# Optimization experiments

Measured on AMD Instinct MI355X. Metric: run time of the kernel, lower is better.

## Reference

```python
import jax, jax.numpy as jnp
import numpy as np

N = 16000   # query points
M = 16000   # support points
NB = 32     # neighbors per query
A = 4       # kanchor (SO(2)/z-axis discrete anchors, kanchor<10 branch)
K = 15      # kernel points
CIN = 32
COUT = 32
RADIUS = 1.0
KP_EXTENT = 0.6


def _make_kernel_points(key):
    # KPConv-style kernel points inside a sphere of radius 0.66*RADIUS, first point at center
    kp = jax.random.normal(key, (K, 3), dtype=jnp.float32)
    kp = kp / (jnp.linalg.norm(kp, axis=-1, keepdims=True) + 1e-8)
    r = jax.random.uniform(jax.random.fold_in(key, 1), (K, 1), dtype=jnp.float32) ** (1.0 / 3.0)
    kp = kp * r * (0.66 * RADIUS)
    return kp.at[0].set(0.0)


def _make_anchors():
    # kanchor=4 -> rotations about z by 2*pi*a/A (E2PN get_anchors for kanchor<10)
    ang = 2.0 * jnp.pi * jnp.arange(A, dtype=jnp.float32) / A
    c, s = jnp.cos(ang), jnp.sin(ang)
    z = jnp.zeros_like(c)
    o = jnp.ones_like(c)
    return jnp.stack([c, -s, z, s, c, z, z, z, o], axis=-1).reshape(A, 3, 3)


def setup_inputs() -> dict:
    key = jax.random.key(0)
    k1, k2, k3, k4, k5, k6 = jax.random.split(key, 6)
    q_pts = jax.random.uniform(k1, (N, 3), dtype=jnp.float32) * 0.5
    s_pts = jax.random.uniform(k2, (M, 3), dtype=jnp.float32) * 0.5
    neighb_inds = jax.random.randint(k3, (N, NB), 0, M, dtype=jnp.int32)
    x = jax.random.normal(k4, (M, A, CIN), dtype=jnp.float32)
    kernel_points = _make_kernel_points(k5)
    anchors = _make_anchors()
    # kaiming-uniform-ish init of the (K, C_in, C_out) separable conv weights
    bound = float(np.sqrt(6.0 / ((1 + 5) * CIN)))
    weights = jax.random.uniform(k6, (K, CIN, COUT), dtype=jnp.float32,
                                 minval=-bound, maxval=bound)
    return {"q_pts": q_pts, "s_pts": s_pts, "neighb_inds": neighb_inds, "x": x,
            "kernel_points": kernel_points, "anchors": anchors, "weights": weights}


def reference(q_pts, s_pts, neighb_inds, x, kernel_points, anchors, weights):
    # neighbor gather, centered on query points: [N, NB, 3]
    neighbors = s_pts[neighb_inds] - q_pts[:, None, :]
    # rotate kernel points by each anchor: [A, K, 3]
    rot_kp = jnp.einsum('aij,kj->aki', anchors, kernel_points)
    # squared distances via |n|^2 + |kp|^2 - 2 n.kp (avoids [A,N,NB,K,3] blowup)
    n2 = jnp.sum(neighbors * neighbors, axis=-1)          # [N, NB]
    k2 = jnp.sum(rot_kp * rot_kp, axis=-1)                # [A, K]
    cross = jnp.einsum('nbj,akj->anbk', neighbors, rot_kp)
    sq_distances = n2[None, :, :, None] + k2[:, None, None, :] - 2.0 * cross  # [A,N,NB,K]
    # linear KP influence, clamped at 0
    all_weights = jnp.clip(1.0 - jnp.sqrt(jnp.maximum(sq_distances, 1e-12)) / KP_EXTENT,
                           0.0, None)                      # [A, N, NB, K]
    # gather neighbor features: [N, NB, A, C_in]
    neighb_x = x[neighb_inds]
    # weight neighbors onto kernel points (sum aggregation): [A, N, K, C_in]
    weighted_feats = jnp.einsum('anbk,nbac->ankc', all_weights, neighb_x)
    # per-kernel-point small GEMMs, summed over K: [N, A, C_out]
    out = jnp.einsum('ankc,kcd->nad', weighted_feats, weights)
    return out
```

## Files before the change

### kernel.cpp

```cpp
#include <hip/hip_runtime.h>


typedef short bf16x8 __attribute__((ext_vector_type(8)));
typedef float f32x4  __attribute__((ext_vector_type(4)));

__device__ __forceinline__ unsigned short f2bf(float f) {
    unsigned u = __builtin_bit_cast(unsigned, f);
    return (unsigned short)((u + 0x8000u) >> 16);
}

__device__ __forceinline__ unsigned pack2bf(float hi, float lo) {
    unsigned uh = __builtin_bit_cast(unsigned, hi) + 0x8000u;
    unsigned ul = __builtin_bit_cast(unsigned, lo) + 0x8000u;
    return __builtin_amdgcn_perm(uh, ul, 0x07060302u);
}

__global__ void prep_w(const float* __restrict__ W, unsigned short* __restrict__ Wp) {
    const int idx = blockIdx.x * 256 + threadIdx.x;
    const int kk = idx >> 10, d = (idx >> 5) & 31, e = idx & 31;
    const int kcs = kk * 32 + e;
    const int c = kcs >> 4, k = kcs & 15;
    const float v = (k < 15) ? W[(k * 32 + c) * 32 + d] : 0.0f;
    Wp[idx] = f2bf(v);
}

__global__ void prep_x(const float* __restrict__ x, unsigned short* __restrict__ xb) {
    const int i = (blockIdx.x * 256 + threadIdx.x) * 8;
    const float4 v0 = *(const float4*)&x[i];
    const float4 v1 = *(const float4*)&x[i + 4];
    uint4 u;
    u.x = pack2bf(v0.y, v0.x); u.y = pack2bf(v0.w, v0.z);
    u.z = pack2bf(v1.y, v1.x); u.w = pack2bf(v1.w, v1.z);
    *(uint4*)&xb[i] = u;
}

__global__ __launch_bounds__(256) void kpconv_mfma(
    const float* __restrict__ q_pts,
    const float* __restrict__ s_pts,
    const int*   __restrict__ inds,
    const unsigned short* __restrict__ xb,
    const float* __restrict__ kp,
    const float* __restrict__ anchors,
    const unsigned short* __restrict__ Wp,
    float*       __restrict__ out)
{
    __shared__ __align__(16) unsigned short xa_s[16384];
    __shared__ __align__(16) float nbr[576];
    __shared__ __align__(16) float rk_s[256];

    const int t  = threadIdx.x;
    const int n0 = blockIdx.x * 4;

    {
        const int c4 = t & 7, bg = (t >> 3) & 7, q = t >> 6;
        const int4 rows = *(const int4*)&inds[(n0 + q) * 32 + 4 * bg];
        const int fc  = c4 & 3;
        const int bb  = 4 * (bg & 1);
        const int blk = 8 * ((bg >> 1) ^ fc);
        unsigned short* base = &xa_s[(q * 32) * 32 + blk + bb];
        #pragma unroll
        for (int a = 0; a < 4; ++a) {
            const uint2 r0 = *(const uint2*)&xb[rows.x * 128 + a * 32 + c4 * 4];
            const uint2 r1 = *(const uint2*)&xb[rows.y * 128 + a * 32 + c4 * 4];
            const uint2 r2 = *(const uint2*)&xb[rows.z * 128 + a * 32 + c4 * 4];
            const uint2 r3 = *(const uint2*)&xb[rows.w * 128 + a * 32 + c4 * 4];
            unsigned short* pa = base + a * 4096;
            uint2 w;
            w.x = __builtin_amdgcn_perm(r1.x, r0.x, 0x05040100u);
            w.y = __builtin_amdgcn_perm(r3.x, r2.x, 0x05040100u);
            *(uint2*)&pa[(4 * c4 + 0) * 32] = w;
            w.x = __builtin_amdgcn_perm(r1.x, r0.x, 0x07060302u);
            w.y = __builtin_amdgcn_perm(r3.x, r2.x, 0x07060302u);
            *(uint2*)&pa[(4 * c4 + 1) * 32] = w;
            w.x = __builtin_amdgcn_perm(r1.y, r0.y, 0x05040100u);
            w.y = __builtin_amdgcn_perm(r3.y, r2.y, 0x05040100u);
            *(uint2*)&pa[(4 * c4 + 2) * 32] = w;
            w.x = __builtin_amdgcn_perm(r1.y, r0.y, 0x07060302u);
            w.y = __builtin_amdgcn_perm(r3.y, r2.y, 0x07060302u);
            *(uint2*)&pa[(4 * c4 + 3) * 32] = w;
        }
    }

    if (t < 128) {
        const int q = t >> 5, b = t & 31;
        const int idx = inds[(n0 + q) * 32 + b];
        const float qx = q_pts[(n0 + q) * 3 + 0];
        const float qy = q_pts[(n0 + q) * 3 + 1];
        const float qz = q_pts[(n0 + q) * 3 + 2];
        const float nx = s_pts[idx * 3 + 0] - qx;
        const float ny = s_pts[idx * 3 + 1] - qy;
        const float nz = s_pts[idx * 3 + 2] - qz;
        float4 v; v.x = nx; v.y = ny; v.z = nz; v.w = nx*nx + ny*ny + nz*nz;
        *(float4*)&nbr[(q * 36 + b + (b >> 3)) * 4] = v;
    } else if (t < 192) {
        const int j = t - 128;
        const int a = j >> 4, k = j & 15;
        float4 v;
        if (k < 15) {
            const float kx = kp[k*3+0], ky = kp[k*3+1], kz = kp[k*3+2];
            const float* R = anchors + a * 9;
            v.x = R[0]*kx + R[1]*ky + R[2]*kz;
            v.y = R[3]*kx + R[4]*ky + R[5]*kz;
            v.z = R[6]*kx + R[7]*ky + R[8]*kz;
            v.w = v.x*v.x + v.y*v.y + v.z*v.z;
        } else {
            v.x = 0.0f; v.y = 0.0f; v.z = 0.0f; v.w = 1e30f;
        }
        *(float4*)&rk_s[(a * 16 + k) * 4] = v;
    }
    __syncthreads();

    const int a    = t >> 6;
    const int lane = t & 63;
    const int l15  = lane & 15;
    const int quad = lane >> 4;
    const int fc   = (l15 >> 2) & 3;

    const float4 r4 = *(const float4*)&rk_s[(a * 16 + l15) * 4];
    unsigned short* wfb = &xa_s[a * 4096];

    #pragma unroll
    for (int q = 0; q < 4; ++q) {
        float w8[8];
        #pragma unroll
        for (int j = 0; j < 8; ++j) {
            const int b = quad * 8 + j;
            const float4 nb = *(const float4*)&nbr[(q * 36 + b + (b >> 3)) * 4];
            const float dot = fmaf(nb.x, r4.x, fmaf(nb.y, r4.y, nb.z * r4.z));
            const float sq  = fmaf(-2.0f, dot, nb.w + r4.w);
            const float d   = sqrtf(fmaxf(sq, 1e-12f));
            w8[j] = fmaxf(fmaf(d, -(1.0f / 0.6f), 1.0f), 0.0f);
        }
        uint4 uu;
        uu.x = pack2bf(w8[1], w8[0]); uu.y = pack2bf(w8[3], w8[2]);
        uu.z = pack2bf(w8[5], w8[4]); uu.w = pack2bf(w8[7], w8[6]);
        const bf16x8 afr = __builtin_bit_cast(bf16x8, uu);

        const bf16x8 b0 = *(const bf16x8*)&xa_s[((a*4 + q)*32 + l15)      * 32 + 8 * (quad ^ fc)];
        const bf16x8 b1 = *(const bf16x8*)&xa_s[((a*4 + q)*32 + l15 + 16) * 32 + 8 * (quad ^ fc)];
        f32x4 d0 = {0.f,0.f,0.f,0.f}, d1 = {0.f,0.f,0.f,0.f};
        d0 = __builtin_amdgcn_mfma_f32_16x16x32_bf16(afr, b0, d0, 0, 0, 0);
        d1 = __builtin_amdgcn_mfma_f32_16x16x32_bf16(afr, b1, d1, 0, 0, 0);
        uint2 s0, s1;
        s0.x = pack2bf(d0[1], d0[0]); s0.y = pack2bf(d0[3], d0[2]);
        s1.x = pack2bf(d1[1], d1[0]); s1.y = pack2bf(d1[3], d1[2]);
        *(uint2*)&wfb[q*512 + (( l15       * 16 + quad * 4) ^ (q * 16))] = s0;
        *(uint2*)&wfb[q*512 + (((l15 + 16) * 16 + quad * 4) ^ (q * 16))] = s1;
    }

    const int qq = l15 & 3;
    f32x4 o0 = {0.f,0.f,0.f,0.f}, o1 = {0.f,0.f,0.f,0.f};
    #pragma unroll
    for (int kk = 0; kk < 16; ++kk) {
        const bf16x8 a2 = *(const bf16x8*)&wfb[qq*512 + ((kk*32 + quad*8) ^ (qq*16))];
        const bf16x8 w0 = *(const bf16x8*)&Wp[kk*1024 + l15*32 + quad*8];
        const bf16x8 w1 = *(const bf16x8*)&Wp[kk*1024 + (l15+16)*32 + quad*8];
        o0 = __builtin_amdgcn_mfma_f32_16x16x32_bf16(a2, w0, o0, 0, 0, 0);
        o1 = __builtin_amdgcn_mfma_f32_16x16x32_bf16(a2, w1, o1, 0, 0, 0);
    }
    if (quad == 0) {
        #pragma unroll
        for (int r = 0; r < 4; ++r) {
            out[((n0 + r) * 4 + a) * 32 + l15]      = o0[r];
            out[((n0 + r) * 4 + a) * 32 + 16 + l15] = o1[r];
        }
    }
}

extern "C" void kernel_launch(void* const* d_in, const int* in_sizes, int n_in,
                              void* d_out, int out_size, void* d_ws, size_t ws_size,
                              hipStream_t stream) {
    const float* q_pts   = (const float*)d_in[0];
    const float* s_pts   = (const float*)d_in[1];
    const int*   inds    = (const int*)d_in[2];
    const float* x       = (const float*)d_in[3];
    const float* kp      = (const float*)d_in[4];
    const float* anchors = (const float*)d_in[5];
    const float* weights = (const float*)d_in[6];
    float*       out     = (float*)d_out;

    unsigned short* Wp = (unsigned short*)d_ws;
    unsigned short* xb = (unsigned short*)((char*)d_ws + (1 << 16));

    prep_w<<<dim3(64),   dim3(256), 0, stream>>>(weights, Wp);
    prep_x<<<dim3(1000), dim3(256), 0, stream>>>(x, xb);
    kpconv_mfma<<<dim3(4000), dim3(256), 0, stream>>>(
        q_pts, s_pts, inds, xb, kp, anchors, Wp, out);
}
```

Measured before the change: 123.8 us.

## Process four query groups per block with register-prefetched gathers

Each block now handles 16 query points in four groups of four. The neighbor-feature and point gathers for the next group are issued into registers before the current group's MFMA work, so global gather latency overlaps compute. The rotated kernel points are computed once per block, and the grid shrinks from 4000 to 1000 blocks. The trade-offs are higher register pressure from the 16-entry prefetch buffer, fewer blocks to spread across CUs, and an extra barrier per group.

```diff
diff --git a/kernel.cpp b/kernel.cpp
--- a/kernel.cpp
+++ b/kernel.cpp
@@ -48,57 +48,24 @@
     __shared__ __align__(16) float nbr[576];
     __shared__ __align__(16) float rk_s[256];
 
-    const int t  = threadIdx.x;
-    const int n0 = blockIdx.x * 4;
-
-    {
-        const int c4 = t & 7, bg = (t >> 3) & 7, q = t >> 6;
-        const int4 rows = *(const int4*)&inds[(n0 + q) * 32 + 4 * bg];
-        const int fc  = c4 & 3;
-        const int bb  = 4 * (bg & 1);
-        const int blk = 8 * ((bg >> 1) ^ fc);
-        unsigned short* base = &xa_s[(q * 32) * 32 + blk + bb];
-        #pragma unroll
-        for (int a = 0; a < 4; ++a) {
-            const uint2 r0 = *(const uint2*)&xb[rows.x * 128 + a * 32 + c4 * 4];
-            const uint2 r1 = *(const uint2*)&xb[rows.y * 128 + a * 32 + c4 * 4];
-            const uint2 r2 = *(const uint2*)&xb[rows.z * 128 + a * 32 + c4 * 4];
-            const uint2 r3 = *(const uint2*)&xb[rows.w * 128 + a * 32 + c4 * 4];
-            unsigned short* pa = base + a * 4096;
-            uint2 w;
-            w.x = __builtin_amdgcn_perm(r1.x, r0.x, 0x05040100u);
-            w.y = __builtin_amdgcn_perm(r3.x, r2.x, 0x05040100u);
-            *(uint2*)&pa[(4 * c4 + 0) * 32] = w;
-            w.x = __builtin_amdgcn_perm(r1.x, r0.x, 0x07060302u);
-            w.y = __builtin_amdgcn_perm(r3.x, r2.x, 0x07060302u);
-            *(uint2*)&pa[(4 * c4 + 1) * 32] = w;
-            w.x = __builtin_amdgcn_perm(r1.y, r0.y, 0x05040100u);
-            w.y = __builtin_amdgcn_perm(r3.y, r2.y, 0x05040100u);
-            *(uint2*)&pa[(4 * c4 + 2) * 32] = w;
-            w.x = __builtin_amdgcn_perm(r1.y, r0.y, 0x07060302u);
-            w.y = __builtin_amdgcn_perm(r3.y, r2.y, 0x07060302u);
-            *(uint2*)&pa[(4 * c4 + 3) * 32] = w;
-        }
-    }
-
-    if (t < 128) {
-        const int q = t >> 5, b = t & 31;
-        const int idx = inds[(n0 + q) * 32 + b];
-        const float qx = q_pts[(n0 + q) * 3 + 0];
-        const float qy = q_pts[(n0 + q) * 3 + 1];
-        const float qz = q_pts[(n0 + q) * 3 + 2];
-        const float nx = s_pts[idx * 3 + 0] - qx;
-        const float ny = s_pts[idx * 3 + 1] - qy;
-        const float nz = s_pts[idx * 3 + 2] - qz;
-        float4 v; v.x = nx; v.y = ny; v.z = nz; v.w = nx*nx + ny*ny + nz*nz;
-        *(float4*)&nbr[(q * 36 + b + (b >> 3)) * 4] = v;
-    } else if (t < 192) {
+    const int t    = threadIdx.x;
+    const int nblk = blockIdx.x * 16;
+
+    const int c4 = t & 7, bg = (t >> 3) & 7, qg = t >> 6;
+    const int a = t >> 6, lane = t & 63, l15 = lane & 15, quad = lane >> 4;
+    const int fc = (l15 >> 2) & 3;
+
+    uint2 gb[16];
+    int   pidx = 0;
+    float psx = 0, psy = 0, psz = 0, pqx = 0, pqy = 0, pqz = 0;
+
+    if (t >= 128 && t < 192) {
         const int j = t - 128;
-        const int a = j >> 4, k = j & 15;
+        const int aa = j >> 4, k = j & 15;
         float4 v;
         if (k < 15) {
             const float kx = kp[k*3+0], ky = kp[k*3+1], kz = kp[k*3+2];
-            const float* R = anchors + a * 9;
+            const float* R = anchors + aa * 9;
             v.x = R[0]*kx + R[1]*ky + R[2]*kz;
             v.y = R[3]*kx + R[4]*ky + R[5]*kz;
             v.z = R[6]*kx + R[7]*ky + R[8]*kz;
@@ -106,64 +73,128 @@
         } else {
             v.x = 0.0f; v.y = 0.0f; v.z = 0.0f; v.w = 1e30f;
         }
-        *(float4*)&rk_s[(a * 16 + k) * 4] = v;
+        *(float4*)&rk_s[(aa * 16 + k) * 4] = v;
     }
-    __syncthreads();
-
-    const int a    = t >> 6;
-    const int lane = t & 63;
-    const int l15  = lane & 15;
-    const int quad = lane >> 4;
-    const int fc   = (l15 >> 2) & 3;
-
-    const float4 r4 = *(const float4*)&rk_s[(a * 16 + l15) * 4];
-    unsigned short* wfb = &xa_s[a * 4096];
+    {
+        const int4 rows = *(const int4*)&inds[(nblk + qg) * 32 + 4 * bg];
+        #pragma unroll
+        for (int aa = 0; aa < 4; ++aa) {
+            gb[aa*4+0] = *(const uint2*)&xb[rows.x * 128 + aa * 32 + c4 * 4];
+            gb[aa*4+1] = *(const uint2*)&xb[rows.y * 128 + aa * 32 + c4 * 4];
+            gb[aa*4+2] = *(const uint2*)&xb[rows.z * 128 + aa * 32 + c4 * 4];
+            gb[aa*4+3] = *(const uint2*)&xb[rows.w * 128 + aa * 32 + c4 * 4];
+        }
+        if (t < 128) {
+            const int qq2 = t >> 5, b = t & 31;
+            pidx = inds[(nblk + qq2) * 32 + b];
+            psx = s_pts[pidx*3+0]; psy = s_pts[pidx*3+1]; psz = s_pts[pidx*3+2];
+            pqx = q_pts[(nblk+qq2)*3+0]; pqy = q_pts[(nblk+qq2)*3+1]; pqz = q_pts[(nblk+qq2)*3+2];
+        }
+    }
 
     #pragma unroll
-    for (int q = 0; q < 4; ++q) {
-        float w8[8];
+    for (int g = 0; g < 4; ++g) {
+        const int n0 = nblk + g * 4;
+
+        if (t < 128) {
+            const int qq2 = t >> 5, b = t & 31;
+            const float nx = psx - pqx, ny = psy - pqy, nz = psz - pqz;
+            float4 v; v.x = nx; v.y = ny; v.z = nz; v.w = nx*nx + ny*ny + nz*nz;
+            *(float4*)&nbr[(qq2 * 36 + b + (b >> 3)) * 4] = v;
+        }
+        {
+            const int bb  = 4 * (bg & 1);
+            const int blk = 8 * ((bg >> 1) ^ (c4 & 3));
+            unsigned short* base = &xa_s[(qg * 32) * 32 + blk + bb];
+            #pragma unroll
+            for (int aa = 0; aa < 4; ++aa) {
+                unsigned short* pa = base + aa * 4096;
+                uint2 w;
+                w.x = __builtin_amdgcn_perm(gb[aa*4+1].x, gb[aa*4+0].x, 0x05040100u);
+                w.y = __builtin_amdgcn_perm(gb[aa*4+3].x, gb[aa*4+2].x, 0x05040100u);
+                *(uint2*)&pa[(4 * c4 + 0) * 32] = w;
+                w.x = __builtin_amdgcn_perm(gb[aa*4+1].x, gb[aa*4+0].x, 0x07060302u);
+                w.y = __builtin_amdgcn_perm(gb[aa*4+3].x, gb[aa*4+2].x, 0x07060302u);
+                *(uint2*)&pa[(4 * c4 + 1) * 32] = w;
+                w.x = __builtin_amdgcn_perm(gb[aa*4+1].y, gb[aa*4+0].y, 0x05040100u);
+                w.y = __builtin_amdgcn_perm(gb[aa*4+3].y, gb[aa*4+2].y, 0x05040100u);
+                *(uint2*)&pa[(4 * c4 + 2) * 32] = w;
+                w.x = __builtin_amdgcn_perm(gb[aa*4+1].y, gb[aa*4+0].y, 0x07060302u);
+                w.y = __builtin_amdgcn_perm(gb[aa*4+3].y, gb[aa*4+2].y, 0x07060302u);
+                *(uint2*)&pa[(4 * c4 + 3) * 32] = w;
+            }
+        }
+        __syncthreads();
+
+        if (g < 3) {
+            const int n1 = n0 + 4;
+            const int4 rows = *(const int4*)&inds[(n1 + qg) * 32 + 4 * bg];
+            #pragma unroll
+            for (int aa = 0; aa < 4; ++aa) {
+                gb[aa*4+0] = *(const uint2*)&xb[rows.x * 128 + aa * 32 + c4 * 4];
+                gb[aa*4+1] = *(const uint2*)&xb[rows.y * 128 + aa * 32 + c4 * 4];
+                gb[aa*4+2] = *(const uint2*)&xb[rows.z * 128 + aa * 32 + c4 * 4];
+                gb[aa*4+3] = *(const uint2*)&xb[rows.w * 128 + aa * 32 + c4 * 4];
+            }
+            if (t < 128) {
+                const int qq2 = t >> 5, b = t & 31;
+                pidx = inds[(n1 + qq2) * 32 + b];
+                psx = s_pts[pidx*3+0]; psy = s_pts[pidx*3+1]; psz = s_pts[pidx*3+2];
+                pqx = q_pts[(n1+qq2)*3+0]; pqy = q_pts[(n1+qq2)*3+1]; pqz = q_pts[(n1+qq2)*3+2];
+            }
+        }
+
+        const float4 r4 = *(const float4*)&rk_s[(a * 16 + l15) * 4];
+        unsigned short* wfb = &xa_s[a * 4096];
+
         #pragma unroll
-        for (int j = 0; j < 8; ++j) {
-            const int b = quad * 8 + j;
-            const float4 nb = *(const float4*)&nbr[(q * 36 + b + (b >> 3)) * 4];
-            const float dot = fmaf(nb.x, r4.x, fmaf(nb.y, r4.y, nb.z * r4.z));
-            const float sq  = fmaf(-2.0f, dot, nb.w + r4.w);
-            const float d   = sqrtf(fmaxf(sq, 1e-12f));
-            w8[j] = fmaxf(fmaf(d, -(1.0f / 0.6f), 1.0f), 0.0f);
-        }
-        uint4 uu;
-        uu.x = pack2bf(w8[1], w8[0]); uu.y = pack2bf(w8[3], w8[2]);
-        uu.z = pack2bf(w8[5], w8[4]); uu.w = pack2bf(w8[7], w8[6]);
-        const bf16x8 afr = __builtin_bit_cast(bf16x8, uu);
-
-        const bf16x8 b0 = *(const bf16x8*)&xa_s[((a*4 + q)*32 + l15)      * 32 + 8 * (quad ^ fc)];
-        const bf16x8 b1 = *(const bf16x8*)&xa_s[((a*4 + q)*32 + l15 + 16) * 32 + 8 * (quad ^ fc)];
-        f32x4 d0 = {0.f,0.f,0.f,0.f}, d1 = {0.f,0.f,0.f,0.f};
-        d0 = __builtin_amdgcn_mfma_f32_16x16x32_bf16(afr, b0, d0, 0, 0, 0);
-        d1 = __builtin_amdgcn_mfma_f32_16x16x32_bf16(afr, b1, d1, 0, 0, 0);
-        uint2 s0, s1;
-        s0.x = pack2bf(d0[1], d0[0]); s0.y = pack2bf(d0[3], d0[2]);
-        s1.x = pack2bf(d1[1], d1[0]); s1.y = pack2bf(d1[3], d1[2]);
-        *(uint2*)&wfb[q*512 + (( l15       * 16 + quad * 4) ^ (q * 16))] = s0;
-        *(uint2*)&wfb[q*512 + (((l15 + 16) * 16 + quad * 4) ^ (q * 16))] = s1;
-    }
-
-    const int qq = l15 & 3;
-    f32x4 o0 = {0.f,0.f,0.f,0.f}, o1 = {0.f,0.f,0.f,0.f};
-    #pragma unroll
-    for (int kk = 0; kk < 16; ++kk) {
-        const bf16x8 a2 = *(const bf16x8*)&wfb[qq*512 + ((kk*32 + quad*8) ^ (qq*16))];
-        const bf16x8 w0 = *(const bf16x8*)&Wp[kk*1024 + l15*32 + quad*8];
-        const bf16x8 w1 = *(const bf16x8*)&Wp[kk*1024 + (l15+16)*32 + quad*8];
-        o0 = __builtin_amdgcn_mfma_f32_16x16x32_bf16(a2, w0, o0, 0, 0, 0);
-        o1 = __builtin_amdgcn_mfma_f32_16x16x32_bf16(a2, w1, o1, 0, 0, 0);
-    }
-    if (quad == 0) {
+        for (int q = 0; q < 4; ++q) {
+            float w8[8];
+            #pragma unroll
+            for (int j = 0; j < 8; ++j) {
+                const int b = quad * 8 + j;
+                const float4 nb = *(const float4*)&nbr[(q * 36 + b + (b >> 3)) * 4];
+                const float dot = fmaf(nb.x, r4.x, fmaf(nb.y, r4.y, nb.z * r4.z));
+                const float sq  = fmaf(-2.0f, dot, nb.w + r4.w);
+                const float d   = sqrtf(fmaxf(sq, 1e-12f));
+                w8[j] = fmaxf(fmaf(d, -(1.0f / 0.6f), 1.0f), 0.0f);
+            }
+            uint4 uu;
+            uu.x = pack2bf(w8[1], w8[0]); uu.y = pack2bf(w8[3], w8[2]);
+            uu.z = pack2bf(w8[5], w8[4]); uu.w = pack2bf(w8[7], w8[6]);
+            const bf16x8 afr = __builtin_bit_cast(bf16x8, uu);
+
+            const bf16x8 b0 = *(const bf16x8*)&xa_s[((a*4 + q)*32 + l15)      * 32 + 8 * (quad ^ fc)];
+            const bf16x8 b1 = *(const bf16x8*)&xa_s[((a*4 + q)*32 + l15 + 16) * 32 + 8 * (quad ^ fc)];
+            f32x4 d0 = {0.f,0.f,0.f,0.f}, d1 = {0.f,0.f,0.f,0.f};
+            d0 = __builtin_amdgcn_mfma_f32_16x16x32_bf16(afr, b0, d0, 0, 0, 0);
+            d1 = __builtin_amdgcn_mfma_f32_16x16x32_bf16(afr, b1, d1, 0, 0, 0);
+            uint2 s0, s1;
+            s0.x = pack2bf(d0[1], d0[0]); s0.y = pack2bf(d0[3], d0[2]);
+            s1.x = pack2bf(d1[1], d1[0]); s1.y = pack2bf(d1[3], d1[2]);
+            *(uint2*)&wfb[q*512 + (( l15       * 16 + quad * 4) ^ (q * 16))] = s0;
+            *(uint2*)&wfb[q*512 + (((l15 + 16) * 16 + quad * 4) ^ (q * 16))] = s1;
+        }
+
+        const int qq = l15 & 3;
+        f32x4 o0 = {0.f,0.f,0.f,0.f}, o1 = {0.f,0.f,0.f,0.f};
         #pragma unroll
-        for (int r = 0; r < 4; ++r) {
-            out[((n0 + r) * 4 + a) * 32 + l15]      = o0[r];
-            out[((n0 + r) * 4 + a) * 32 + 16 + l15] = o1[r];
-        }
+        for (int kk = 0; kk < 16; ++kk) {
+            const bf16x8 a2 = *(const bf16x8*)&wfb[qq*512 + ((kk*32 + quad*8) ^ (qq*16))];
+            const bf16x8 w0 = *(const bf16x8*)&Wp[kk*1024 + l15*32 + quad*8];
+            const bf16x8 w1 = *(const bf16x8*)&Wp[kk*1024 + (l15+16)*32 + quad*8];
+            o0 = __builtin_amdgcn_mfma_f32_16x16x32_bf16(a2, w0, o0, 0, 0, 0);
+            o1 = __builtin_amdgcn_mfma_f32_16x16x32_bf16(a2, w1, o1, 0, 0, 0);
+        }
+        if (quad == 0) {
+            #pragma unroll
+            for (int r = 0; r < 4; ++r) {
+                out[((n0 + r) * 4 + a) * 32 + l15]      = o0[r];
+                out[((n0 + r) * 4 + a) * 32 + 16 + l15] = o1[r];
+            }
+        }
+
+        if (g < 3) __syncthreads();
     }
 }
 
@@ -184,6 +215,6 @@
 
     prep_w<<<dim3(64),   dim3(256), 0, stream>>>(weights, Wp);
     prep_x<<<dim3(1000), dim3(256), 0, stream>>>(x, xb);
-    kpconv_mfma<<<dim3(4000), dim3(256), 0, stream>>>(
+    kpconv_mfma<<<dim3(1000), dim3(256), 0, stream>>>(
         q_pts, s_pts, inds, xb, kp, anchors, Wp, out);
 }
```

Measured after the change: 133.4 us. +7.7%, slower.

## Compute KP squared distances with split-bf16 MFMA instead of scalar FMAs

Applied to the files above, without the earlier changes.

Each neighbour's coordinates and squared norm, and each rotated kernel point's coordinates and squared norm, are split into high and low bf16 parts. These are packed so that a single 16x16x32 bf16 MFMA produces n2 + k2 - 2·n·kp for 16 neighbours by 16 kernel points. This replaces the per-lane scalar dot-product loop and the rk_s/nbr float LDS staging. The neighbour-to-lane ordering of the MFMA output differs from before, so the swizzle of the gathered feature layout is changed to match. The hi/lo split keeps roughly fp32 accuracy, but it adds packing work and some precision risk where near-cancelling distances pass through the sqrt.

```diff
diff --git a/kernel.cpp b/kernel.cpp
--- a/kernel.cpp
+++ b/kernel.cpp
@@ -8,11 +8,17 @@
     unsigned u = __builtin_bit_cast(unsigned, f);
     return (unsigned short)((u + 0x8000u) >> 16);
 }
-
+__device__ __forceinline__ float bf2f(unsigned short h) {
+    return __builtin_bit_cast(float, (unsigned)h << 16);
+}
 __device__ __forceinline__ unsigned pack2bf(float hi, float lo) {
     unsigned uh = __builtin_bit_cast(unsigned, hi) + 0x8000u;
     unsigned ul = __builtin_bit_cast(unsigned, lo) + 0x8000u;
     return __builtin_amdgcn_perm(uh, ul, 0x07060302u);
+}
+__device__ __forceinline__ void bfsplit(float v, unsigned short& h, unsigned short& l) {
+    h = f2bf(v);
+    l = f2bf(v - bf2f(h));
 }
 
 __global__ void prep_w(const float* __restrict__ W, unsigned short* __restrict__ Wp) {
@@ -45,26 +51,87 @@
     float*       __restrict__ out)
 {
     __shared__ __align__(16) unsigned short xa_s[16384];
-    __shared__ __align__(16) float nbr[576];
-    __shared__ __align__(16) float rk_s[256];
+    __shared__ __align__(16) unsigned short nbr32[3072];
+    __shared__ __align__(16) unsigned short zz[128];
 
     const int t  = threadIdx.x;
     const int n0 = blockIdx.x * 4;
+    const int a = t >> 6, lane = t & 63, l15 = lane & 15, quad = lane >> 4;
+
+    bf16x8 rkb;
+    {
+        float rx = 0.f, ry = 0.f, rz = 0.f, k2 = 1e30f;
+        if (l15 < 15) {
+            const float kx = kp[l15*3+0], ky = kp[l15*3+1], kz = kp[l15*3+2];
+            const float* R = anchors + a * 9;
+            rx = R[0]*kx + R[1]*ky + R[2]*kz;
+            ry = R[3]*kx + R[4]*ky + R[5]*kz;
+            rz = R[6]*kx + R[7]*ky + R[8]*kz;
+            k2 = rx*rx + ry*ry + rz*rz;
+        }
+        unsigned short k2h,k2l, Rxh,Rxl, Ryh,Ryl, Rzh,Rzl;
+        bfsplit(k2, k2h, k2l);
+        bfsplit(-2.0f*rx, Rxh, Rxl);
+        bfsplit(-2.0f*ry, Ryh, Ryl);
+        bfsplit(-2.0f*rz, Rzh, Rzl);
+        const unsigned ONE = 0x3F80u;
+        uint4 u;
+        if (quad == 0) {
+            u.x = (unsigned)k2h | ((unsigned)k2l << 16);
+            u.y = (unsigned)Rxh | ((unsigned)Rxl << 16);
+            u.z = (unsigned)Rxh | ((unsigned)Ryh << 16);
+            u.w = (unsigned)Ryl | ((unsigned)Ryh << 16);
+        } else if (quad == 1) {
+            u.x = (unsigned)Rzh | ((unsigned)Rzl << 16);
+            u.y = (unsigned)Rzh | (ONE << 16);
+            u.z = ONE;
+            u.w = 0u;
+        } else {
+            u.x = u.y = u.z = u.w = 0u;
+        }
+        rkb = __builtin_bit_cast(bf16x8, u);
+    }
+
+    if (t < 128) {
+        const int q = t >> 5, b = t & 31;
+        const int idx = inds[(n0 + q) * 32 + b];
+        const float nx = s_pts[idx*3+0] - q_pts[(n0+q)*3+0];
+        const float ny = s_pts[idx*3+1] - q_pts[(n0+q)*3+1];
+        const float nz = s_pts[idx*3+2] - q_pts[(n0+q)*3+2];
+        const float n2 = nx*nx + ny*ny + nz*nz;
+        unsigned short nxh,nxl, nyh,nyl, nzh,nzl, n2h,n2l;
+        bfsplit(nx, nxh, nxl); bfsplit(ny, nyh, nyl);
+        bfsplit(nz, nzh, nzl); bfsplit(n2, n2h, n2l);
+        const unsigned ONE = 0x3F80u;
+        uint4 lo, hi;
+        lo.x = ONE | (ONE << 16);
+        lo.y = (unsigned)nxh | ((unsigned)nxh << 16);
+        lo.z = (unsigned)nxl | ((unsigned)nyh << 16);
+        lo.w = (unsigned)nyh | ((unsigned)nyl << 16);
+        hi.x = (unsigned)nzh | ((unsigned)nzh << 16);
+        hi.y = (unsigned)nzl | ((unsigned)n2h << 16);
+        hi.z = (unsigned)n2l;
+        hi.w = 0u;
+        unsigned short* p = &nbr32[(q * 32 + b) * 24];
+        *(uint4*)(p)     = lo;
+        *(uint4*)(p + 8) = hi;
+    } else if (t < 144) {
+        *(uint4*)&zz[(t - 128) * 8] = make_uint4(0,0,0,0);
+    }
 
     {
         const int c4 = t & 7, bg = (t >> 3) & 7, q = t >> 6;
         const int4 rows = *(const int4*)&inds[(n0 + q) * 32 + 4 * bg];
-        const int fc  = c4 & 3;
-        const int bb  = 4 * (bg & 1);
-        const int blk = 8 * ((bg >> 1) ^ fc);
-        unsigned short* base = &xa_s[(q * 32) * 32 + blk + bb];
+        const int fcs   = c4 & 3;
+        const int slotb = ((bg & 3) ^ fcs) * 8 + (bg >> 2) * 4;
+        unsigned short* base = &xa_s[(q * 32) * 32 + slotb];
         #pragma unroll
-        for (int a = 0; a < 4; ++a) {
-            const uint2 r0 = *(const uint2*)&xb[rows.x * 128 + a * 32 + c4 * 4];
-            const uint2 r1 = *(const uint2*)&xb[rows.y * 128 + a * 32 + c4 * 4];
-            const uint2 r2 = *(const uint2*)&xb[rows.z * 128 + a * 32 + c4 * 4];
-            const uint2 r3 = *(const uint2*)&xb[rows.w * 128 + a * 32 + c4 * 4];
-            unsigned short* pa = base + a * 4096;
+        for (int aa = 0; aa < 4; ++aa) {
+            const uint2 r0 = *(const uint2*)&xb[rows.x * 128 + aa * 32 + c4 * 4];
+            const uint2 r1 = *(const uint2*)&xb[rows.y * 128 + aa * 32 + c4 * 4];
+            const uint2 r2 = *(const uint2*)&xb[rows.z * 128 + aa * 32 + c4 * 4];
+            const uint2 r3 = *(const uint2*)&xb[rows.w * 128 + aa * 32 + c4 * 4];
+            unsigned short* pa = base + aa * 4096;
             uint2 w;
             w.x = __builtin_amdgcn_perm(r1.x, r0.x, 0x05040100u);
             w.y = __builtin_amdgcn_perm(r3.x, r2.x, 0x05040100u);
@@ -80,56 +147,25 @@
             *(uint2*)&pa[(4 * c4 + 3) * 32] = w;
         }
     }
-
-    if (t < 128) {
-        const int q = t >> 5, b = t & 31;
-        const int idx = inds[(n0 + q) * 32 + b];
-        const float qx = q_pts[(n0 + q) * 3 + 0];
-        const float qy = q_pts[(n0 + q) * 3 + 1];
-        const float qz = q_pts[(n0 + q) * 3 + 2];
-        const float nx = s_pts[idx * 3 + 0] - qx;
-        const float ny = s_pts[idx * 3 + 1] - qy;
-        const float nz = s_pts[idx * 3 + 2] - qz;
-        float4 v; v.x = nx; v.y = ny; v.z = nz; v.w = nx*nx + ny*ny + nz*nz;
-        *(float4*)&nbr[(q * 36 + b + (b >> 3)) * 4] = v;
-    } else if (t < 192) {
-        const int j = t - 128;
-        const int a = j >> 4, k = j & 15;
-        float4 v;
-        if (k < 15) {
-            const float kx = kp[k*3+0], ky = kp[k*3+1], kz = kp[k*3+2];
-            const float* R = anchors + a * 9;
-            v.x = R[0]*kx + R[1]*ky + R[2]*kz;
-            v.y = R[3]*kx + R[4]*ky + R[5]*kz;
-            v.z = R[6]*kx + R[7]*ky + R[8]*kz;
-            v.w = v.x*v.x + v.y*v.y + v.z*v.z;
-        } else {
-            v.x = 0.0f; v.y = 0.0f; v.z = 0.0f; v.w = 1e30f;
-        }
-        *(float4*)&rk_s[(a * 16 + k) * 4] = v;
-    }
     __syncthreads();
 
-    const int a    = t >> 6;
-    const int lane = t & 63;
-    const int l15  = lane & 15;
-    const int quad = lane >> 4;
-    const int fc   = (l15 >> 2) & 3;
-
-    const float4 r4 = *(const float4*)&rk_s[(a * 16 + l15) * 4];
+    const int fc = (l15 >> 2) & 3;
     unsigned short* wfb = &xa_s[a * 4096];
+    const f32x4 zacc = {0.f, 0.f, 0.f, 0.f};
 
     #pragma unroll
     for (int q = 0; q < 4; ++q) {
+        const unsigned short* aX = (quad < 2)
+            ? &nbr32[(q * 32 + l15) * 24 + (quad & 1) * 8]       : &zz[l15 * 8];
+        const unsigned short* aY = (quad < 2)
+            ? &nbr32[(q * 32 + 16 + l15) * 24 + (quad & 1) * 8]  : &zz[l15 * 8];
+        const f32x4 s0 = __builtin_amdgcn_mfma_f32_16x16x32_bf16(*(const bf16x8*)aX, rkb, zacc, 0, 0, 0);
+        const f32x4 s1 = __builtin_amdgcn_mfma_f32_16x16x32_bf16(*(const bf16x8*)aY, rkb, zacc, 0, 0, 0);
         float w8[8];
         #pragma unroll
-        for (int j = 0; j < 8; ++j) {
-            const int b = quad * 8 + j;
-            const float4 nb = *(const float4*)&nbr[(q * 36 + b + (b >> 3)) * 4];
-            const float dot = fmaf(nb.x, r4.x, fmaf(nb.y, r4.y, nb.z * r4.z));
-            const float sq  = fmaf(-2.0f, dot, nb.w + r4.w);
-            const float d   = sqrtf(fmaxf(sq, 1e-12f));
-            w8[j] = fmaxf(fmaf(d, -(1.0f / 0.6f), 1.0f), 0.0f);
+        for (int j = 0; j < 4; ++j) {
+            w8[j]     = fmaxf(fmaf(sqrtf(fmaxf(s0[j], 1e-12f)), -1.6666667f, 1.0f), 0.0f);
+            w8[4 + j] = fmaxf(fmaf(sqrtf(fmaxf(s1[j], 1e-12f)), -1.6666667f, 1.0f), 0.0f);
         }
         uint4 uu;
         uu.x = pack2bf(w8[1], w8[0]); uu.y = pack2bf(w8[3], w8[2]);
@@ -138,18 +174,18 @@
 
         const bf16x8 b0 = *(const bf16x8*)&xa_s[((a*4 + q)*32 + l15)      * 32 + 8 * (quad ^ fc)];
         const bf16x8 b1 = *(const bf16x8*)&xa_s[((a*4 + q)*32 + l15 + 16) * 32 + 8 * (quad ^ fc)];
-        f32x4 d0 = {0.f,0.f,0.f,0.f}, d1 = {0.f,0.f,0.f,0.f};
+        f32x4 d0 = zacc, d1 = zacc;
         d0 = __builtin_amdgcn_mfma_f32_16x16x32_bf16(afr, b0, d0, 0, 0, 0);
         d1 = __builtin_amdgcn_mfma_f32_16x16x32_bf16(afr, b1, d1, 0, 0, 0);
-        uint2 s0, s1;
-        s0.x = pack2bf(d0[1], d0[0]); s0.y = pack2bf(d0[3], d0[2]);
-        s1.x = pack2bf(d1[1], d1[0]); s1.y = pack2bf(d1[3], d1[2]);
-        *(uint2*)&wfb[q*512 + (( l15       * 16 + quad * 4) ^ (q * 16))] = s0;
-        *(uint2*)&wfb[q*512 + (((l15 + 16) * 16 + quad * 4) ^ (q * 16))] = s1;
+        uint2 s0p, s1p;
+        s0p.x = pack2bf(d0[1], d0[0]); s0p.y = pack2bf(d0[3], d0[2]);
+        s1p.x = pack2bf(d1[1], d1[0]); s1p.y = pack2bf(d1[3], d1[2]);
+        *(uint2*)&wfb[q*512 + (( l15       * 16 + quad * 4) ^ (q * 16))] = s0p;
+        *(uint2*)&wfb[q*512 + (((l15 + 16) * 16 + quad * 4) ^ (q * 16))] = s1p;
     }
 
     const int qq = l15 & 3;
-    f32x4 o0 = {0.f,0.f,0.f,0.f}, o1 = {0.f,0.f,0.f,0.f};
+    f32x4 o0 = zacc, o1 = zacc;
     #pragma unroll
     for (int kk = 0; kk < 16; ++kk) {
         const bf16x8 a2 = *(const bf16x8*)&wfb[qq*512 + ((kk*32 + quad*8) ^ (qq*16))];
```

Measured after the change: 123.6 us. No clear change (-0.2%).
